# Kernel tuning notes

Measured on AMD Instinct MI355X. Metric: run time of the kernel, lower is better.

Reference implementation:

```python
import jax, jax.numpy as jnp
import numpy as np

N_HEAD = 16


def setup_inputs() -> dict:
    key = jax.random.key(0)
    ks = jax.random.split(key, 5)
    B, L, C = 2, 2048, 1024
    s = 0.02
    return {
        "x": jax.random.normal(ks[0], (B, L, C), dtype=jnp.float32),
        "attn_mask": jnp.ones((B, L), dtype=jnp.int64),
        "Wq": jax.random.normal(ks[1], (C, C), dtype=jnp.float32) * s,
        "Wk": jax.random.normal(ks[2], (C, C), dtype=jnp.float32) * s,
        "Wv": jax.random.normal(ks[3], (C, C), dtype=jnp.float32) * s,
        "Wp": jax.random.normal(ks[4], (C, C), dtype=jnp.float32) * s,
    }


def reference(x, attn_mask, Wq, Wk, Wv, Wp):
    B, L, C = x.shape
    H = N_HEAD
    D = C // H
    # nn.Linear(bias=False): y = x @ W.T with W of shape (out, in)
    q = (x @ Wq.T).reshape(B, L, H, D).transpose(0, 2, 1, 3)  # (B,H,L,D)
    k = (x @ Wk.T).reshape(B, L, H, D).transpose(0, 2, 1, 3)
    v = (x @ Wv.T).reshape(B, L, H, D).transpose(0, 2, 1, 3)
    att = jnp.einsum("bhqd,bhkd->bhqk", q, k) / jnp.sqrt(jnp.asarray(D, x.dtype))
    causal = jnp.tril(jnp.ones((L, L), dtype=bool))  # (L,L)
    tok = (attn_mask != 0)[:, None, None, :]  # (B,1,1,L) key-side padding mask
    mask = causal[None, None, :, :] & tok
    att = jnp.where(mask, att, -jnp.inf)
    att = jax.nn.softmax(att, axis=-1)
    # dropout p=0.0 (eval): identity
    y = jnp.einsum("bhqk,bhkd->bhqd", att, v)
    y = y.transpose(0, 2, 1, 3).reshape(B, L, C)
    return y @ Wp.T
```

## Files before the change

### kernel.cpp

```cpp
#include <hip/hip_runtime.h>
#include <hip/hip_bf16.h>
#include <cstdint>

typedef _Float16 f16;
typedef _Float16 f16x4 __attribute__((ext_vector_type(4)));
typedef _Float16 f16x8 __attribute__((ext_vector_type(8)));
typedef float f32x4 __attribute__((ext_vector_type(4)));

#define LNEG (-1e30f)

__device__ __forceinline__ f32x4 mfma16(f16x8 a, f16x8 b, f32x4 c){
    return __builtin_amdgcn_mfma_f32_16x16x32_f16(a, b, c, 0, 0, 0);
}

__global__ void cvt_f32_f16(const float* __restrict__ in, f16* __restrict__ out, int n4){
    int i = blockIdx.x * blockDim.x + threadIdx.x;
    if (i < n4){
        float4 v = ((const float4*)in)[i];
        f16x4 o = { (f16)v.x, (f16)v.y, (f16)v.z, (f16)v.w };
        *(f16x4*)&out[(size_t)i * 4] = o;
    }
}

template<typename OutT>
__global__ __launch_bounds__(256) void gemm_xwt(
    const f16* __restrict__ A, const f16* __restrict__ W0, size_t wstride,
    OutT* __restrict__ out0, size_t ostride, int M, int N, int K)
{
    const int tid  = threadIdx.x;
    const int lane = tid & 63;
    const int w    = tid >> 6;
    const int wr   = w >> 1, wc = w & 1;
    const int m0   = blockIdx.y * 128;
    const int n0   = blockIdx.x * 128;
    const f16* Wz  = W0 + wstride * blockIdx.z;
    OutT* out      = out0 + ostride * blockIdx.z;

    __shared__ f16 At[128 * 64];
    __shared__ f16 Bt[128 * 64];

    f32x4 acc[4][4] = {};

    for (int k0 = 0; k0 < K; k0 += 64){
        #pragma unroll
        for (int j = 0; j < 4; ++j){
            int off  = (j * 256 + tid) * 16;
            int row  = off >> 7;
            int colb = off & 127;
            int swz  = row * 128 + (colb ^ ((row & 7) << 4));
            f16x8 av = *(const f16x8*)&A [(size_t)(m0 + row) * K + k0 + (colb >> 1)];
            *(f16x8*)((char*)At + swz) = av;
            f16x8 bv = *(const f16x8*)&Wz[(size_t)(n0 + row) * K + k0 + (colb >> 1)];
            *(f16x8*)((char*)Bt + swz) = bv;
        }
        __syncthreads();
        #pragma unroll
        for (int kk = 0; kk < 2; ++kk){
            f16x8 af[4], bf[4];
            #pragma unroll
            for (int mf = 0; mf < 4; ++mf){
                int row = wr * 64 + mf * 16 + (lane & 15);
                int cb  = (kk * 64 + 16 * (lane >> 4)) ^ ((row & 7) << 4);
                af[mf] = *(const f16x8*)((const char*)At + row * 128 + cb);
            }
            #pragma unroll
            for (int nf = 0; nf < 4; ++nf){
                int row = wc * 64 + nf * 16 + (lane & 15);
                int cb  = (kk * 64 + 16 * (lane >> 4)) ^ ((row & 7) << 4);
                bf[nf] = *(const f16x8*)((const char*)Bt + row * 128 + cb);
            }
            #pragma unroll
            for (int mf = 0; mf < 4; ++mf)
                #pragma unroll
                for (int nf = 0; nf < 4; ++nf)
                    acc[mf][nf] = mfma16(af[mf], bf[nf], acc[mf][nf]);
        }
        __syncthreads();
    }
    #pragma unroll
    for (int mf = 0; mf < 4; ++mf)
        #pragma unroll
        for (int nf = 0; nf < 4; ++nf)
            #pragma unroll
            for (int r = 0; r < 4; ++r){
                int row = m0 + wr * 64 + mf * 16 + 4 * (lane >> 4) + r;
                int col = n0 + wc * 64 + nf * 16 + (lane & 15);
                out[(size_t)row * N + col] = (OutT)acc[mf][nf][r];
            }
}

__global__ __launch_bounds__(256) void transpose_v(const f16* __restrict__ v, f16* __restrict__ vt){
    const int t  = threadIdx.x;
    const int lt = blockIdx.x;
    const int bh = blockIdx.y;
    const int b  = bh >> 4, h = bh & 15;
    const int l0 = lt * 64;
    __shared__ f16 tile[64][72];
    #pragma unroll
    for (int r = 0; r < 2; ++r){
        int i  = t / 8 + 32 * r;
        int jb = t % 8;
        f16x8 vv = *(const f16x8*)&v[(size_t)(b * 2048 + l0 + i) * 1024 + h * 64 + jb * 8];
        *(f16x8*)&tile[i][jb * 8] = vv;
    }
    __syncthreads();
    #pragma unroll
    for (int r = 0; r < 2; ++r){
        int d  = t / 8 + 32 * r;
        int lb = t % 8;
        f16x8 o;
        #pragma unroll
        for (int q2 = 0; q2 < 8; ++q2) o[q2] = tile[lb * 8 + q2][d];
        *(f16x8*)&vt[(size_t)(bh * 64 + d) * 2048 + l0 + lb * 8] = o;
    }
}

__global__ __launch_bounds__(256, 4) void attn_fused(
    const f16* __restrict__ q, const f16* __restrict__ k,
    const f16* __restrict__ vt, const int* __restrict__ amask,
    f16* __restrict__ y)
{
    const int tid  = threadIdx.x;
    const int lane = tid & 63;
    const int w    = tid >> 6;
    const int g    = lane >> 4;
    const int qq   = lane & 15;

    const int lin = blockIdx.x;
    const int jj = lin >> 8, ii = lin & 255;
    const int qt = (jj & 1) ? (31 - (ii & 31)) : (ii & 31);
    const int bh = (ii >> 5) | (jj << 3);
    const int b = bh >> 4, h = bh & 15;
    const int q0w = qt * 64 + w * 16;
    const int nkt = qt + 1;

    __shared__ char sK[2][64 * 128];
    __shared__ char sV[2][64 * 128];
    __shared__ char sP[4][16 * 128];

    const int srow = (tid * 2) >> 3;
    const int sc8a = (tid * 2) & 7, sc8b = sc8a + 1;
    const int swka = (sc8a * 16) ^ ((srow & 7) << 4);
    const int swkb = (sc8b * 16) ^ ((srow & 7) << 4);
    const f16* kbase  = k  + ((size_t)b * 2048) * 1024 + h * 64;
    const f16* vtbase = vt + (size_t)bh * 64 * 2048;

    f16x8 aq[2];
    #pragma unroll
    for (int f = 0; f < 2; ++f){
        aq[f] = *(const f16x8*)&q[((size_t)(b * 2048 + q0w + qq)) * 1024 + h * 64 + f * 32 + 8 * g];
        #pragma unroll
        for (int j = 0; j < 8; ++j) aq[f][j] *= (f16)0.125f;
    }

    f32x4 acc_o[4] = {};
    float m_ln = LNEG, l_ln = 0.f;

    {
        f16x8 ka  = *(const f16x8*)(kbase  + (size_t)srow * 1024 + sc8a * 8);
        f16x8 kb2 = *(const f16x8*)(kbase  + (size_t)srow * 1024 + sc8b * 8);
        f16x8 va  = *(const f16x8*)(vtbase + (size_t)srow * 2048 + sc8a * 8);
        f16x8 vb  = *(const f16x8*)(vtbase + (size_t)srow * 2048 + sc8b * 8);
        *(f16x8*)(sK[0] + srow * 128 + swka) = ka;
        *(f16x8*)(sK[0] + srow * 128 + swkb) = kb2;
        *(f16x8*)(sV[0] + srow * 128 + swka) = va;
        *(f16x8*)(sV[0] + srow * 128 + swkb) = vb;
    }
    __syncthreads();

    for (int kt = 0; kt < nkt; ++kt){
        const int cur = kt & 1;
        const int k0 = kt * 64;
        const bool pre = (kt + 1 < nkt);

        f16x8 ka, kb2, va, vb;
        if (pre){
            const int nk0 = k0 + 64;
            ka  = *(const f16x8*)(kbase  + (size_t)(nk0 + srow) * 1024 + sc8a * 8);
            kb2 = *(const f16x8*)(kbase  + (size_t)(nk0 + srow) * 1024 + sc8b * 8);
            va  = *(const f16x8*)(vtbase + (size_t)srow * 2048 + nk0 + sc8a * 8);
            vb  = *(const f16x8*)(vtbase + (size_t)srow * 2048 + nk0 + sc8b * 8);
        }

        unsigned long long tokbits = __ballot(amask[b * 2048 + k0 + lane] != 0);
        const bool tokall = (tokbits == ~0ull);

        f32x4 acc_s[4] = {};
        #pragma unroll
        for (int kf = 0; kf < 4; ++kf){
            const int keyl = kf * 16 + qq;
            const char* kr = sK[cur] + keyl * 128;
            const int sw = (keyl & 7) << 4;
            #pragma unroll
            for (int f = 0; f < 2; ++f){
                f16x8 ak = *(const f16x8*)(kr + ((f * 64 + 16 * g) ^ sw));
                acc_s[kf] = mfma16(ak, aq[f], acc_s[kf]);
            }
        }

        const bool fullt = (k0 + 63 <= q0w) && tokall;
        float sv[16];
        #pragma unroll
        for (int kf = 0; kf < 4; ++kf)
            #pragma unroll
            for (int r = 0; r < 4; ++r){
                float s = acc_s[kf][r];
                if (!fullt){
                    const int keyl = kf * 16 + 4 * g + r;
                    const bool ok = (k0 + keyl <= q0w + qq) && ((tokbits >> keyl) & 1);
                    s = ok ? s : LNEG;
                }
                sv[kf * 4 + r] = s;
            }

        float tmax = sv[0];
        #pragma unroll
        for (int i = 1; i < 16; ++i) tmax = fmaxf(tmax, sv[i]);
        tmax = fmaxf(tmax, __shfl_xor(tmax, 16));
        tmax = fmaxf(tmax, __shfl_xor(tmax, 32));
        const bool skip = __all(tmax <= m_ln + 5.f);
        float alpha = 1.f;
        if (!skip){
            const float newm = fmaxf(m_ln, tmax);
            alpha = __expf(m_ln - newm);
            m_ln = newm;
        }
        float rs = 0.f;
        float pr[16];
        #pragma unroll
        for (int i = 0; i < 16; ++i){ pr[i] = __expf(sv[i] - m_ln); rs += pr[i]; }
        rs += __shfl_xor(rs, 16);
        rs += __shfl_xor(rs, 32);
        l_ln = l_ln * alpha + rs;
        if (!skip){
            #pragma unroll
            for (int r = 0; r < 4; ++r){
                const float ar = __shfl(alpha, 4 * g + r);
                #pragma unroll
                for (int nf = 0; nf < 4; ++nf) acc_o[nf][r] *= ar;
            }
        }

        char* pbase = sP[w] + qq * 128;
        const int swp = (qq & 7) << 4;
        #pragma unroll
        for (int kf = 0; kf < 4; ++kf){
            f16x4 pk = { (f16)pr[kf*4+0], (f16)pr[kf*4+1], (f16)pr[kf*4+2], (f16)pr[kf*4+3] };
            *(f16x4*)(pbase + ((kf * 32 + 8 * g) ^ swp)) = pk;
        }

        #pragma unroll
        for (int f = 0; f < 2; ++f){
            f16x8 ap = *(const f16x8*)(pbase + ((f * 64 + 16 * g) ^ swp));
            #pragma unroll
            for (int nf = 0; nf < 4; ++nf){
                const int d = nf * 16 + qq;
                f16x8 bv = *(const f16x8*)(sV[cur] + d * 128 + ((f * 64 + 16 * g) ^ ((d & 7) << 4)));
                acc_o[nf] = mfma16(ap, bv, acc_o[nf]);
            }
        }

        if (pre){
            const int nb = cur ^ 1;
            *(f16x8*)(sK[nb] + srow * 128 + swka) = ka;
            *(f16x8*)(sK[nb] + srow * 128 + swkb) = kb2;
            *(f16x8*)(sV[nb] + srow * 128 + swka) = va;
            *(f16x8*)(sV[nb] + srow * 128 + swkb) = vb;
        }
        __syncthreads();
    }

    const float invl = 1.f / l_ln;
    #pragma unroll
    for (int r = 0; r < 4; ++r){
        const float ir = __shfl(invl, 4 * g + r);
        const int row = q0w + 4 * g + r;
        #pragma unroll
        for (int nf = 0; nf < 4; ++nf)
            y[((size_t)(b * 2048 + row)) * 1024 + h * 64 + nf * 16 + qq] = (f16)(acc_o[nf][r] * ir);
    }
}

extern "C" void kernel_launch(void* const* d_in, const int* in_sizes, int n_in,
                              void* d_out, int out_size, void* d_ws, size_t ws_size,
                              hipStream_t stream){
    const float* x  = (const float*)d_in[0];
    const int*   am = (const int*)d_in[1];
    const float* Wq = (const float*)d_in[2];
    const float* Wk = (const float*)d_in[3];
    const float* Wv = (const float*)d_in[4];
    const float* Wp = (const float*)d_in[5];
    float* out = (float*)d_out;

    char* ws = (char*)d_ws;
    const size_t XE = (size_t)4096 * 1024;
    const size_t WE = (size_t)1024 * 1024;

    f16* x16 = (f16*)(ws);
    f16* w16 = (f16*)(ws + XE * 2);
    f16* qkv = (f16*)(ws + XE * 2 + WE * 8);
    f16* vt  = (f16*)(ws + XE * 2 + WE * 8 + XE * 6);
    f16* y16 = (f16*)(ws + XE * 2 + WE * 8 + XE * 8);

    cvt_f32_f16<<<(int)(XE / 4 / 256), 256, 0, stream>>>(x,  x16,          (int)(XE / 4));
    cvt_f32_f16<<<(int)(WE / 4 / 256), 256, 0, stream>>>(Wq, w16 + 0 * WE, (int)(WE / 4));
    cvt_f32_f16<<<(int)(WE / 4 / 256), 256, 0, stream>>>(Wk, w16 + 1 * WE, (int)(WE / 4));
    cvt_f32_f16<<<(int)(WE / 4 / 256), 256, 0, stream>>>(Wv, w16 + 2 * WE, (int)(WE / 4));
    cvt_f32_f16<<<(int)(WE / 4 / 256), 256, 0, stream>>>(Wp, w16 + 3 * WE, (int)(WE / 4));

    gemm_xwt<f16><<<dim3(8, 32, 3), 256, 0, stream>>>(x16, w16, WE, qkv, XE, 4096, 1024, 1024);

    transpose_v<<<dim3(32, 32), 256, 0, stream>>>(qkv + 2 * XE, vt);

    attn_fused<<<dim3(1024), 256, 0, stream>>>(qkv, qkv + XE, vt, am, y16);

    gemm_xwt<float><<<dim3(8, 32, 1), 256, 0, stream>>>(y16, w16 + 3 * WE, 0, out, 0, 4096, 1024, 1024);
}
```

Baseline: 132.9 us.

## Fuse conversion launches, use direct global-to-LDS loads, exp2 softmax, MFMA priority hints

The five fp32-to-fp16 conversion launches are merged into one kernel that picks its source by index. The GEMM staging now uses global_load_lds to write tiles straight into LDS without passing through registers, and drops the XOR swizzle, which may bring back LDS bank conflicts on the fragment reads. In attention, the log2(e) factor is folded into the Q scale so softmax uses exp2, and the rescale-skip threshold is raised from 5 to 8. s_setprio hints are placed around the MFMA blocks.

```diff
diff --git a/kernel.cpp b/kernel.cpp
--- a/kernel.cpp
+++ b/kernel.cpp
@@ -13,23 +13,40 @@
     return __builtin_amdgcn_mfma_f32_16x16x32_f16(a, b, c, 0, 0, 0);
 }
 
-__global__ void cvt_f32_f16(const float* __restrict__ in, f16* __restrict__ out, int n4){
+__device__ __forceinline__ void gload16(const void* g, void* l){
+    __builtin_amdgcn_global_load_lds((const __attribute__((address_space(1))) void*)g,
+                                     (__attribute__((address_space(3))) void*)l,
+                                     16, 0, 0);
+}
+
+__global__ __launch_bounds__(256) void cvt5(
+    const float* __restrict__ x,  const float* __restrict__ wq,
+    const float* __restrict__ wk, const float* __restrict__ wv,
+    const float* __restrict__ wp, f16* __restrict__ dst, int nx4, int nw4)
+{
     int i = blockIdx.x * blockDim.x + threadIdx.x;
-    if (i < n4){
-        float4 v = ((const float4*)in)[i];
-        f16x4 o = { (f16)v.x, (f16)v.y, (f16)v.z, (f16)v.w };
-        *(f16x4*)&out[(size_t)i * 4] = o;
-    }
+    const float* src; int off;
+    if (i < nx4){ src = x; off = i; }
+    else {
+        int j = i - nx4;
+        int s = j >> 18;
+        off = j & (nw4 - 1);
+        src = (s == 0) ? wq : (s == 1) ? wk : (s == 2) ? wv : wp;
+    }
+    float4 v = ((const float4*)src)[off];
+    f16x4 o = { (f16)v.x, (f16)v.y, (f16)v.z, (f16)v.w };
+    *(f16x4*)&dst[(size_t)i * 4] = o;
 }
 
 template<typename OutT>
-__global__ __launch_bounds__(256) void gemm_xwt(
+__global__ __launch_bounds__(256) void gemm_m97(
     const f16* __restrict__ A, const f16* __restrict__ W0, size_t wstride,
     OutT* __restrict__ out0, size_t ostride, int M, int N, int K)
 {
     const int tid  = threadIdx.x;
     const int lane = tid & 63;
     const int w    = tid >> 6;
+    const int g    = lane >> 4;
     const int wr   = w >> 1, wc = w & 1;
     const int m0   = blockIdx.y * 128;
     const int n0   = blockIdx.x * 128;
@@ -41,17 +58,16 @@
 
     f32x4 acc[4][4] = {};
 
+    const int lrow = lane >> 3;
+    const int lcol = (lane & 7) * 8;
+
     for (int k0 = 0; k0 < K; k0 += 64){
         #pragma unroll
         for (int j = 0; j < 4; ++j){
-            int off  = (j * 256 + tid) * 16;
-            int row  = off >> 7;
-            int colb = off & 127;
-            int swz  = row * 128 + (colb ^ ((row & 7) << 4));
-            f16x8 av = *(const f16x8*)&A [(size_t)(m0 + row) * K + k0 + (colb >> 1)];
-            *(f16x8*)((char*)At + swz) = av;
-            f16x8 bv = *(const f16x8*)&Wz[(size_t)(n0 + row) * K + k0 + (colb >> 1)];
-            *(f16x8*)((char*)Bt + swz) = bv;
+            const int c   = w * 4 + j;
+            const int row = c * 8 + lrow;
+            gload16(&A [(size_t)(m0 + row) * K + k0 + lcol], &At[c * 512]);
+            gload16(&Wz[(size_t)(n0 + row) * K + k0 + lcol], &Bt[c * 512]);
         }
         __syncthreads();
         #pragma unroll
@@ -60,14 +76,12 @@
             #pragma unroll
             for (int mf = 0; mf < 4; ++mf){
                 int row = wr * 64 + mf * 16 + (lane & 15);
-                int cb  = (kk * 64 + 16 * (lane >> 4)) ^ ((row & 7) << 4);
-                af[mf] = *(const f16x8*)((const char*)At + row * 128 + cb);
+                af[mf] = *(const f16x8*)((const char*)At + row * 128 + kk * 64 + 16 * g);
             }
             #pragma unroll
             for (int nf = 0; nf < 4; ++nf){
                 int row = wc * 64 + nf * 16 + (lane & 15);
-                int cb  = (kk * 64 + 16 * (lane >> 4)) ^ ((row & 7) << 4);
-                bf[nf] = *(const f16x8*)((const char*)Bt + row * 128 + cb);
+                bf[nf] = *(const f16x8*)((const char*)Bt + row * 128 + kk * 64 + 16 * g);
             }
             #pragma unroll
             for (int mf = 0; mf < 4; ++mf)
@@ -145,12 +159,13 @@
     const f16* kbase  = k  + ((size_t)b * 2048) * 1024 + h * 64;
     const f16* vtbase = vt + (size_t)bh * 64 * 2048;
 
+    const f16 qscale = (f16)(0.125f * 1.44269504088896f);
     f16x8 aq[2];
     #pragma unroll
     for (int f = 0; f < 2; ++f){
         aq[f] = *(const f16x8*)&q[((size_t)(b * 2048 + q0w + qq)) * 1024 + h * 64 + f * 32 + 8 * g];
         #pragma unroll
-        for (int j = 0; j < 8; ++j) aq[f][j] *= (f16)0.125f;
+        for (int j = 0; j < 8; ++j) aq[f][j] *= qscale;
     }
 
     f32x4 acc_o[4] = {};
@@ -186,6 +201,7 @@
         const bool tokall = (tokbits == ~0ull);
 
         f32x4 acc_s[4] = {};
+        __builtin_amdgcn_s_setprio(1);
         #pragma unroll
         for (int kf = 0; kf < 4; ++kf){
             const int keyl = kf * 16 + qq;
@@ -197,6 +213,7 @@
                 acc_s[kf] = mfma16(ak, aq[f], acc_s[kf]);
             }
         }
+        __builtin_amdgcn_s_setprio(0);
 
         const bool fullt = (k0 + 63 <= q0w) && tokall;
         float sv[16];
@@ -218,17 +235,17 @@
         for (int i = 1; i < 16; ++i) tmax = fmaxf(tmax, sv[i]);
         tmax = fmaxf(tmax, __shfl_xor(tmax, 16));
         tmax = fmaxf(tmax, __shfl_xor(tmax, 32));
-        const bool skip = __all(tmax <= m_ln + 5.f);
+        const bool skip = __all(tmax <= m_ln + 8.f);
         float alpha = 1.f;
         if (!skip){
             const float newm = fmaxf(m_ln, tmax);
-            alpha = __expf(m_ln - newm);
+            alpha = exp2f(m_ln - newm);
             m_ln = newm;
         }
         float rs = 0.f;
         float pr[16];
         #pragma unroll
-        for (int i = 0; i < 16; ++i){ pr[i] = __expf(sv[i] - m_ln); rs += pr[i]; }
+        for (int i = 0; i < 16; ++i){ pr[i] = exp2f(sv[i] - m_ln); rs += pr[i]; }
         rs += __shfl_xor(rs, 16);
         rs += __shfl_xor(rs, 32);
         l_ln = l_ln * alpha + rs;
@@ -249,6 +266,8 @@
             *(f16x4*)(pbase + ((kf * 32 + 8 * g) ^ swp)) = pk;
         }
 
+        __builtin_amdgcn_wave_barrier();
+        __builtin_amdgcn_s_setprio(1);
         #pragma unroll
         for (int f = 0; f < 2; ++f){
             f16x8 ap = *(const f16x8*)(pbase + ((f * 64 + 16 * g) ^ swp));
@@ -259,6 +278,7 @@
                 acc_o[nf] = mfma16(ap, bv, acc_o[nf]);
             }
         }
+        __builtin_amdgcn_s_setprio(0);
 
         if (pre){
             const int nb = cur ^ 1;
@@ -302,17 +322,14 @@
     f16* vt  = (f16*)(ws + XE * 2 + WE * 8 + XE * 6);
     f16* y16 = (f16*)(ws + XE * 2 + WE * 8 + XE * 8);
 
-    cvt_f32_f16<<<(int)(XE / 4 / 256), 256, 0, stream>>>(x,  x16,          (int)(XE / 4));
-    cvt_f32_f16<<<(int)(WE / 4 / 256), 256, 0, stream>>>(Wq, w16 + 0 * WE, (int)(WE / 4));
-    cvt_f32_f16<<<(int)(WE / 4 / 256), 256, 0, stream>>>(Wk, w16 + 1 * WE, (int)(WE / 4));
-    cvt_f32_f16<<<(int)(WE / 4 / 256), 256, 0, stream>>>(Wv, w16 + 2 * WE, (int)(WE / 4));
-    cvt_f32_f16<<<(int)(WE / 4 / 256), 256, 0, stream>>>(Wp, w16 + 3 * WE, (int)(WE / 4));
-
-    gemm_xwt<f16><<<dim3(8, 32, 3), 256, 0, stream>>>(x16, w16, WE, qkv, XE, 4096, 1024, 1024);
+    cvt5<<<8192, 256, 0, stream>>>(x, Wq, Wk, Wv, Wp, x16,
+                                   (int)(XE / 4), (int)(WE / 4));
+
+    gemm_m97<f16><<<dim3(8, 32, 3), 256, 0, stream>>>(x16, w16, WE, qkv, XE, 4096, 1024, 1024);
 
     transpose_v<<<dim3(32, 32), 256, 0, stream>>>(qkv + 2 * XE, vt);
 
     attn_fused<<<dim3(1024), 256, 0, stream>>>(qkv, qkv + XE, vt, am, y16);
 
-    gemm_xwt<float><<<dim3(8, 32, 1), 256, 0, stream>>>(y16, w16 + 3 * WE, 0, out, 0, 4096, 1024, 1024);
-}
+    gemm_m97<float><<<dim3(8, 32, 1), 256, 0, stream>>>(y16, w16 + 3 * WE, 0, out, 0, 4096, 1024, 1024);
+}
```

Result: slower. 154.5 us (+16.3%).
